# Optimization experiments

Hardware: AMD Instinct MI355X
Metric: run time of the kernel (lower is better)

## Reference

```python
import jax, jax.numpy as jnp
import numpy as np

B, N, H, IN, OUT = 2, 4096, 64, 32, 8


def setup_inputs() -> dict:
    key = jax.random.key(0)
    ks = jax.random.split(key, 18)
    sc = 0.1  # xavier-ish scale for H=64
    mask = lambda k: (jax.random.uniform(k, (1, N, N)) < 0.1).astype(jnp.float32)
    return {
        "x0": jax.random.normal(ks[0], (B, N, IN), jnp.float32),
        "h0": jax.random.normal(ks[1], (B, N, H), jnp.float32),
        "h1": jax.random.normal(ks[2], (B, N, H), jnp.float32),
        "h2": jax.random.normal(ks[3], (B, N, H), jnp.float32),
        "m00": mask(ks[4]), "m20": mask(ks[5]), "m01": mask(ks[6]),
        "m11": mask(ks[7]), "m12": mask(ks[8]), "m22": mask(ks[9]),
        "Wq": jax.random.normal(ks[10], (3, H, H), jnp.float32) * sc,
        "Wk": jax.random.normal(ks[11], (6, H, H), jnp.float32) * sc,
        "Wsu0": jax.random.normal(ks[12], (H, IN + H), jnp.float32) * sc,
        "Wsu12": jax.random.normal(ks[13], (2, H, H), jnp.float32) * sc,
        "Wdt": jax.random.normal(ks[14], (3, H, H), jnp.float32) * sc,
        "bdt": jnp.zeros((3, H), jnp.float32),
        "step_size": jnp.array(1.0, jnp.float32),
        "out_scale": jnp.array(10.0, jnp.float32),
    }


def _cosine_acc(q, keys_and_masks_and_vals):
    # q: [B,N,H]; each entry: (keys [B,Np,H], mask [1,N,Np], vals [B,Np,H])
    qn = q / jnp.linalg.norm(q, axis=2, keepdims=True)
    acc = 0.0
    for k, m, v in keys_and_masks_and_vals:
        kn = k / jnp.linalg.norm(k, axis=2, keepdims=True)
        scale = 1.0 / jnp.sum(m, axis=2, keepdims=True)
        rel = scale * m * jnp.einsum("bnh,bmh->bnm", qn, kn)  # [B,N,Np]
        acc = acc + jnp.einsum("bnm,bmh->bnh", rel, v)
    return acc


def reference(x0, h0, h1, h2, m00, m20, m01, m11, m12, m22,
              Wq, Wk, Wsu0, Wsu12, Wdt, bdt, step_size, out_scale):
    # queries per successor type, keys per edge; edges (pred->succ):
    # 0->0 (k0), 2->0 (k1), 0->1 (k2), 1->1 (k3), 1->2 (k4), 2->2 (k5)
    q0 = h0 @ Wq[0].T
    q1 = h1 @ Wq[1].T
    q2 = h2 @ Wq[2].T
    acc0 = _cosine_acc(q0, [(h0 @ Wk[0].T, m00, h0), (h2 @ Wk[1].T, m20, h2)])
    acc1 = _cosine_acc(q1, [(h0 @ Wk[2].T, m01, h0), (h1 @ Wk[3].T, m11, h1)])
    acc2 = _cosine_acc(q2, [(h1 @ Wk[4].T, m12, h1), (h2 @ Wk[5].T, m22, h2)])

    def step(h, acc_in, Wsu, t):
        dt = 2.0 * jax.nn.sigmoid(h @ Wdt[t].T + bdt[t]) - 1.0
        return h + step_size * dt * (acc_in @ Wsu.T)

    h0n = step(h0, jnp.concatenate([x0, acc0], axis=2), Wsu0, 0)
    h1n = step(h1, acc1, Wsu12[0], 1)
    h2n = step(h2, acc2, Wsu12[1], 2)
    out2 = out_scale * h2n[:, :, :OUT]
    return (out2, h0n, h1n, h2n)
```

## Files before the change

### kernel.cpp

```cpp
#include <hip/hip_runtime.h>

typedef __bf16 bf16;
typedef bf16 bf16x8 __attribute__((ext_vector_type(8)));
typedef float f32x4 __attribute__((ext_vector_type(4)));
typedef unsigned int uint;
typedef uint u32x2 __attribute__((ext_vector_type(2)));
typedef uint u32x4 __attribute__((ext_vector_type(4)));
typedef unsigned short u16x8 __attribute__((ext_vector_type(8)));

constexpr int NT = 4096;

__device__ __forceinline__ bf16x8 ld8f(const float* p) {
    f32x4 a = *(const f32x4*)p;
    f32x4 b = *(const f32x4*)(p + 4);
    bf16x8 v;
    v[0] = (bf16)a[0]; v[1] = (bf16)a[1]; v[2] = (bf16)a[2]; v[3] = (bf16)a[3];
    v[4] = (bf16)b[0]; v[5] = (bf16)b[1]; v[6] = (bf16)b[2]; v[7] = (bf16)b[3];
    return v;
}

__device__ __forceinline__ uint pack2(float a, float b) {
    unsigned short ua = __builtin_bit_cast(unsigned short, (bf16)a);
    unsigned short ub = __builtin_bit_cast(unsigned short, (bf16)b);
    return (uint)ua | ((uint)ub << 16);
}

__global__ __launch_bounds__(256) void prep_kernel(
    const float* __restrict__ h0, const float* __restrict__ h1, const float* __restrict__ h2,
    const float* __restrict__ Wq, const float* __restrict__ Wk,
    const float* __restrict__ m00, const float* __restrict__ m20, const float* __restrict__ m01,
    const float* __restrict__ m11, const float* __restrict__ m12, const float* __restrict__ m22,
    bf16* __restrict__ qn, bf16* __restrict__ kn, bf16* __restrict__ vT,
    uint* __restrict__ mb, float* __restrict__ rs2)
{
    __shared__ __align__(16) unsigned short tlds[4][16][72];
    const int tid = threadIdx.x, wid = tid >> 6, lane = tid & 63;
    const int l15 = lane & 15, quad = lane >> 4;
    const int bx = blockIdx.x;

    if (bx >= 1536) {
        const int mi = bx - 1536;
        const int e = mi >> 10, rb = mi & 1023;
        const int row = rb * 4 + wid;
        const float* masks[6] = {m00, m20, m01, m11, m12, m22};
        const float* mrow = masks[e] + (size_t)row * NT;
        uint lo = 0, hi = 0;
        int cnt = 0;
#pragma unroll 8
        for (int k = 0; k < 64; k++) {
            float m = mrow[64 * k + lane];
            unsigned long long bal = __ballot(m > 0.5f);
            cnt += __popcll(bal);
            if (lane == k) { lo = (uint)bal; hi = (uint)(bal >> 32); }
        }
        if (lane == 0) rs2[e * NT + row] = (float)cnt;
        u32x2 w = {lo, hi};
        ((u32x2*)(mb + (size_t)(e * NT + row) * 128))[lane] = w;
        return;
    }

    const int rt = bx & 127, sl = bx >> 7;
    const int g0 = rt * 64;
    const int grow = g0 + wid * 16 + l15;
    const float* hs[3] = {h0, h1, h2};
    const int predmap[6] = {0, 2, 0, 1, 1, 2};

    if (sl >= 9) {
        const int p = sl - 9;
        bf16x8 af[2];
#pragma unroll
        for (int hc = 0; hc < 2; hc++)
            af[hc] = ld8f(hs[p] + (size_t)grow * 64 + hc * 32 + quad * 8);
#pragma unroll
        for (int hc = 0; hc < 2; hc++)
            *(u16x8*)(&tlds[wid][l15][hc * 32 + quad * 8]) = __builtin_bit_cast(u16x8, af[hc]);
        unsigned short vals[16];
#pragma unroll
        for (int r = 0; r < 16; r++) vals[r] = tlds[wid][r][lane];
        uint us[8];
#pragma unroll
        for (int k = 0; k < 8; k++) us[k] = (uint)vals[2 * k] | ((uint)vals[2 * k + 1] << 16);
        const int gr0 = g0 + wid * 16;
        const int bb = gr0 >> 12, n0 = gr0 & 4095;
        uint* dst = (uint*)(vT + ((size_t)(p * 2 + bb) * 64 + lane) * NT + n0);
        u32x4 w0 = {us[0], us[1], us[2], us[3]};
        u32x4 w1 = {us[4], us[5], us[6], us[7]};
        *(u32x4*)dst = w0;
        *(u32x4*)(dst + 4) = w1;
        return;
    }

    const int pj = sl;
    const float* W = (pj < 3) ? (Wq + pj * 4096) : (Wk + (pj - 3) * 4096);
    const int src = (pj < 3) ? pj : predmap[pj - 3];
    bf16* outp = (pj < 3) ? (qn + (size_t)pj * 2 * NT * 64)
                          : (kn + (size_t)(pj - 3) * 2 * NT * 64);
    bf16x8 af[2];
#pragma unroll
    for (int hc = 0; hc < 2; hc++)
        af[hc] = ld8f(hs[src] + (size_t)grow * 64 + hc * 32 + quad * 8);

    f32x4 s[4];
#pragma unroll
    for (int it = 0; it < 4; it++) {
        f32x4 acc = {0.f, 0.f, 0.f, 0.f};
#pragma unroll
        for (int hc = 0; hc < 2; hc++) {
            bf16x8 wb = ld8f(W + (size_t)(it * 16 + l15) * 64 + hc * 32 + quad * 8);
            acc = __builtin_amdgcn_mfma_f32_16x16x32_bf16(af[hc], wb, acc, 0, 0, 0);
        }
        s[it] = acc;
    }
#pragma unroll
    for (int r = 0; r < 4; r++) {
        float ss = s[0][r] * s[0][r] + s[1][r] * s[1][r] + s[2][r] * s[2][r] + s[3][r] * s[3][r];
        ss += __shfl_xor(ss, 1); ss += __shfl_xor(ss, 2);
        ss += __shfl_xor(ss, 4); ss += __shfl_xor(ss, 8);
        float rn = rsqrtf(ss);
        s[0][r] *= rn; s[1][r] *= rn; s[2][r] *= rn; s[3][r] *= rn;
    }
    const int rowbase = g0 + wid * 16 + quad * 4;
#pragma unroll
    for (int it = 0; it < 4; it++)
#pragma unroll
        for (int r = 0; r < 4; r++)
            outp[(size_t)(rowbase + r) * 64 + it * 16 + l15] = (bf16)s[it][r];
}

template<int JC>
__global__ __launch_bounds__(256, 4) void attn_kernel(
    const bf16* __restrict__ qn, const bf16* __restrict__ kn, const bf16* __restrict__ vT,
    const uint* __restrict__ mb, float* __restrict__ Pacc)
{
    __shared__ __align__(16) bf16 Klds[64][72];
    __shared__ __align__(16) bf16 Vlds[64][72];
    const int tid = threadIdx.x, wid = tid >> 6, lane = tid & 63;
    const int l15 = lane & 15, quad = lane >> 4;
    constexpr int G = 6 * 32 * 2 * JC;
    const int bxr = blockIdx.x;
    const int wg = (bxr & 7) * (G >> 3) + (bxr >> 3);
    const int jcv = wg % JC;
    int r = wg / JC;
    const int b = r & 1; r >>= 1;
    const int qt = r & 31; const int e = r >> 5;
    const int qtypemap[6] = {0, 0, 1, 1, 2, 2};
    const int predmap[6]  = {0, 2, 0, 1, 1, 2};
    const int qtv = qtypemap[e], pv = predmap[e];
    const int qrow0 = qt * 128, wstrip = wid * 32;
    constexpr int JSPAN = NT / JC;
    constexpr int NI = JSPAN / 64;
    const int jbeg = jcv * JSPAN;

    int srow[2], sch[2];
#pragma unroll
    for (int s = 0; s < 2; s++) {
        int u = tid + 256 * s;
        srow[s] = u >> 3; sch[s] = u & 7;
    }
    const bf16* Ksrc = kn + ((size_t)(e * 2 + b) * NT + jbeg) * 64;
    const bf16* Vsrc = vT + (size_t)(pv * 2 + b) * 64 * NT + jbeg;

    bf16x8 Qf[2][2];
#pragma unroll
    for (int mt = 0; mt < 2; mt++)
#pragma unroll
        for (int hc = 0; hc < 2; hc++)
            Qf[mt][hc] = *(const bf16x8*)(qn +
                ((size_t)(qtv * 2 + b) * NT + qrow0 + wstrip + mt * 16 + l15) * 64 +
                hc * 32 + quad * 8);

    f32x4 acc2[4][2];
#pragma unroll
    for (int ht = 0; ht < 4; ht++)
#pragma unroll
        for (int mt = 0; mt < 2; mt++) {
            f32x4 z = {0.f, 0.f, 0.f, 0.f};
            acc2[ht][mt] = z;
        }

    const uint* mbase[2];
#pragma unroll
    for (int mt = 0; mt < 2; mt++)
        mbase[mt] = mb + (size_t)(e * NT + qrow0 + wstrip + mt * 16 + l15) * 128 + (jbeg >> 5);

    u32x4 kreg[2], vreg[2];
#pragma unroll
    for (int s = 0; s < 2; s++) {
        kreg[s] = *(const u32x4*)(Ksrc + (size_t)srow[s] * 64 + sch[s] * 8);
        vreg[s] = *(const u32x4*)(Vsrc + (size_t)srow[s] * NT + sch[s] * 8);
    }
    u32x2 mcur[2], mnxt[2];
#pragma unroll
    for (int mt = 0; mt < 2; mt++) {
        mcur[mt] = *(const u32x2*)(mbase[mt]);
        mnxt[mt] = *(const u32x2*)(mbase[mt] + ((NI > 1) ? 2 : 0));
    }

#pragma unroll 1
    for (int ji = 0; ji < NI; ji++) {
        const int jn = (ji + 1 < NI) ? (ji + 1) * 64 : 0;

        __syncthreads();
#pragma unroll
        for (int s = 0; s < 2; s++) {
            *(u32x4*)(&Klds[srow[s]][sch[s] * 8]) = kreg[s];
            *(u32x4*)(&Vlds[srow[s]][sch[s] * 8]) = vreg[s];
        }
        __syncthreads();

#pragma unroll
        for (int s = 0; s < 2; s++) {
            kreg[s] = *(const u32x4*)(Ksrc + (size_t)(jn + srow[s]) * 64 + sch[s] * 8);
            vreg[s] = *(const u32x4*)(Vsrc + (size_t)srow[s] * NT + jn + sch[s] * 8);
        }
        const int woff2 = (ji + 2 < NI) ? 2 * (ji + 2) : 0;
        u32x2 mtmp[2];
#pragma unroll
        for (int mt = 0; mt < 2; mt++)
            mtmp[mt] = *(const u32x2*)(mbase[mt] + woff2);

        uint Pd[4][2][2];
#pragma unroll
        for (int jt = 0; jt < 4; jt++) {
            bf16x8 aK0 = *(const bf16x8*)(&Klds[jt * 16 + l15][quad * 8]);
            bf16x8 aK1 = *(const bf16x8*)(&Klds[jt * 16 + l15][32 + quad * 8]);
#pragma unroll
            for (int mt = 0; mt < 2; mt++) {
                f32x4 sc = {0.f, 0.f, 0.f, 0.f};
                sc = __builtin_amdgcn_mfma_f32_16x16x32_bf16(aK0, Qf[mt][0], sc, 0, 0, 0);
                sc = __builtin_amdgcn_mfma_f32_16x16x32_bf16(aK1, Qf[mt][1], sc, 0, 0, 0);
                const uint w = (jt < 2) ? mcur[mt].x : mcur[mt].y;
                const int sh = (jt & 1) * 16 + quad * 4;
#pragma unroll
                for (int k = 0; k < 4; k++)
                    sc[k] = ((w >> (sh + k)) & 1u) ? sc[k] : 0.0f;
                Pd[jt][mt][0] = pack2(sc[0], sc[1]);
                Pd[jt][mt][1] = pack2(sc[2], sc[3]);
            }
        }
#pragma unroll
        for (int mt = 0; mt < 2; mt++) { mcur[mt] = mnxt[mt]; mnxt[mt] = mtmp[mt]; }

        uint Bf[2][2][4];
#pragma unroll
        for (int mt = 0; mt < 2; mt++)
#pragma unroll
            for (int c = 0; c < 2; c++)
#pragma unroll
                for (int d = 0; d < 2; d++) {
                    uint x = Pd[2 * c][mt][d];
                    uint y = Pd[2 * c + 1][mt][d];
                    asm("v_permlane32_swap_b32 %0, %1\n\t"
                        "v_permlane16_swap_b32 %0, %1"
                        : "+v"(x), "+v"(y));
                    Bf[mt][c][d]     = x;
                    Bf[mt][c][d + 2] = y;
                }

#pragma unroll
        for (int ht = 0; ht < 4; ht++)
#pragma unroll
            for (int c = 0; c < 2; c++) {
                bf16x8 a = *(const bf16x8*)(&Vlds[ht * 16 + l15][c * 32 + quad * 8]);
#pragma unroll
                for (int mt = 0; mt < 2; mt++) {
                    u32x4 t = {Bf[mt][c][0], Bf[mt][c][1], Bf[mt][c][2], Bf[mt][c][3]};
                    bf16x8 bbv = __builtin_bit_cast(bf16x8, t);
                    acc2[ht][mt] =
                        __builtin_amdgcn_mfma_f32_16x16x32_bf16(a, bbv, acc2[ht][mt], 0, 0, 0);
                }
            }
    }

#pragma unroll
    for (int ht = 0; ht < 4; ht++)
#pragma unroll
        for (int mt = 0; mt < 2; mt++) {
            const int n = qrow0 + wstrip + mt * 16 + l15;
            *(f32x4*)(Pacc + ((((size_t)(jcv * 6 + e) * 2 + b) * NT + n) << 6) +
                      ht * 16 + quad * 4) = acc2[ht][mt];
        }
}

template<int JC>
__global__ __launch_bounds__(256) void update_kernel(
    const float* __restrict__ x0, const float* __restrict__ h0,
    const float* __restrict__ h1, const float* __restrict__ h2,
    const float* __restrict__ Wsu0, const float* __restrict__ Wsu12,
    const float* __restrict__ Wdt, const float* __restrict__ bdt,
    const float* __restrict__ stepp, const float* __restrict__ oscp,
    const float* __restrict__ Pacc, const float* __restrict__ rs2,
    float* __restrict__ dout)
{
    const int tid = threadIdx.x, wid = tid >> 6, lane = tid & 63;
    const int l15 = lane & 15, quad = lane >> 4;
    const int bx = blockIdx.x;
    const int ih = (bx >= 384) ? 1 : 0;
    const int base = bx - ih * 384;
    const int rt = base & 127, t = base >> 7;
    const int g0 = rt * 64;
    const int grow = g0 + wid * 16 + l15;
    const int n = grow & 4095, bb = grow >> 12;
    const float step = *stepp, osc = *oscp;
    const float* hs[3] = {h0, h1, h2};
    const float* __restrict__ ht_base = hs[t];

    bf16x8 afh[2], afacc[2], afx;
#pragma unroll
    for (int hc = 0; hc < 2; hc++)
        afh[hc] = ld8f(ht_base + (size_t)grow * 64 + hc * 32 + quad * 8);
    if (t == 0) afx = ld8f(x0 + (size_t)grow * 32 + quad * 8);

    const float i0 = 1.f / rs2[(size_t)(2 * t) * NT + n];
    const float i1 = 1.f / rs2[(size_t)(2 * t + 1) * NT + n];
#pragma unroll
    for (int hc = 0; hc < 2; hc++) {
        f32x4 S0a = {0.f,0.f,0.f,0.f}, S0b = {0.f,0.f,0.f,0.f};
        f32x4 S1a = {0.f,0.f,0.f,0.f}, S1b = {0.f,0.f,0.f,0.f};
#pragma unroll
        for (int jc = 0; jc < JC; jc++) {
            const float* p0 = Pacc + ((((size_t)(jc * 6 + 2 * t) * 2 + bb) * NT + n) << 6) +
                              hc * 32 + quad * 8;
            const float* p1 = Pacc + ((((size_t)(jc * 6 + 2 * t + 1) * 2 + bb) * NT + n) << 6) +
                              hc * 32 + quad * 8;
            S0a += *(const f32x4*)p0;  S0b += *(const f32x4*)(p0 + 4);
            S1a += *(const f32x4*)p1;  S1b += *(const f32x4*)(p1 + 4);
        }
        bf16x8 v;
#pragma unroll
        for (int j = 0; j < 4; j++) v[j]     = (bf16)(S0a[j] * i0 + S1a[j] * i1);
#pragma unroll
        for (int j = 0; j < 4; j++) v[4 + j] = (bf16)(S0b[j] * i0 + S1b[j] * i1);
        afacc[hc] = v;
    }

#pragma unroll
    for (int ii = 0; ii < 2; ii++) {
        const int it = ih * 2 + ii;
        const float bdtv = bdt[t * 64 + it * 16 + l15];
        f32x4 z = {0.f, 0.f, 0.f, 0.f};
        f32x4 u = {0.f, 0.f, 0.f, 0.f};
#pragma unroll
        for (int hc = 0; hc < 2; hc++) {
            bf16x8 wb = ld8f(Wdt + (size_t)t * 4096 + (size_t)(it * 16 + l15) * 64 + hc * 32 + quad * 8);
            z = __builtin_amdgcn_mfma_f32_16x16x32_bf16(afh[hc], wb, z, 0, 0, 0);
        }
        if (t == 0) {
            bf16x8 w0 = ld8f(Wsu0 + (size_t)(it * 16 + l15) * 96 + quad * 8);
            u = __builtin_amdgcn_mfma_f32_16x16x32_bf16(afx, w0, u, 0, 0, 0);
#pragma unroll
            for (int kc = 0; kc < 2; kc++) {
                bf16x8 wk = ld8f(Wsu0 + (size_t)(it * 16 + l15) * 96 + 32 + kc * 32 + quad * 8);
                u = __builtin_amdgcn_mfma_f32_16x16x32_bf16(afacc[kc], wk, u, 0, 0, 0);
            }
        } else {
#pragma unroll
            for (int kc = 0; kc < 2; kc++) {
                bf16x8 wk = ld8f(Wsu12 + (size_t)(t - 1) * 4096 + (size_t)(it * 16 + l15) * 64 + kc * 32 + quad * 8);
                u = __builtin_amdgcn_mfma_f32_16x16x32_bf16(afacc[kc], wk, u, 0, 0, 0);
            }
        }
        const int colg = it * 16 + l15;
#pragma unroll
        for (int r = 0; r < 4; r++) {
            int row = g0 + wid * 16 + quad * 4 + r;
            float zz = z[r] + bdtv;
            float dtv = 2.f / (1.f + __expf(-zz)) - 1.f;
            float hval = ht_base[(size_t)row * 64 + colg];
            float hn = hval + step * dtv * u[r];
            dout[65536 + (size_t)t * 524288 + (size_t)row * 64 + colg] = hn;
            if (t == 2 && colg < 8)
                dout[(size_t)row * 8 + colg] = osc * hn;
        }
    }
}

extern "C" void kernel_launch(void* const* d_in, const int* in_sizes, int n_in,
                              void* d_out, int out_size, void* d_ws, size_t ws_size,
                              hipStream_t stream) {
    const float* x0   = (const float*)d_in[0];
    const float* h0   = (const float*)d_in[1];
    const float* h1   = (const float*)d_in[2];
    const float* h2   = (const float*)d_in[3];
    const float* m00  = (const float*)d_in[4];
    const float* m20  = (const float*)d_in[5];
    const float* m01  = (const float*)d_in[6];
    const float* m11  = (const float*)d_in[7];
    const float* m12  = (const float*)d_in[8];
    const float* m22  = (const float*)d_in[9];
    const float* Wq   = (const float*)d_in[10];
    const float* Wk   = (const float*)d_in[11];
    const float* Wsu0 = (const float*)d_in[12];
    const float* Wsu12= (const float*)d_in[13];
    const float* Wdt  = (const float*)d_in[14];
    const float* bdt  = (const float*)d_in[15];
    const float* step = (const float*)d_in[16];
    const float* oscl = (const float*)d_in[17];

    bf16* qn  = (bf16*)d_ws;
    bf16* kn  = qn + 1572864;
    bf16* vT  = kn + 3145728;
    uint* mb  = (uint*)(vT + 1572864);
    float* rs2 = (float*)(mb + 3145728);
    float* Pacc = rs2 + 24576;

    auto need = [](size_t jc) { return 25264128 + jc * 12582912; };
    const int JC = (ws_size >= need(4)) ? 4 : ((ws_size >= need(2)) ? 2 : 1);

    prep_kernel<<<7680, 256, 0, stream>>>(h0, h1, h2, Wq, Wk,
                                          m00, m20, m01, m11, m12, m22,
                                          qn, kn, vT, mb, rs2);

    if (JC == 4) {
        attn_kernel<4><<<6 * 32 * 2 * 4, 256, 0, stream>>>(qn, kn, vT, mb, Pacc);
        update_kernel<4><<<768, 256, 0, stream>>>(x0, h0, h1, h2, Wsu0, Wsu12, Wdt, bdt,
                                                  step, oscl, Pacc, rs2, (float*)d_out);
    } else if (JC == 2) {
        attn_kernel<2><<<6 * 32 * 2 * 2, 256, 0, stream>>>(qn, kn, vT, mb, Pacc);
        update_kernel<2><<<768, 256, 0, stream>>>(x0, h0, h1, h2, Wsu0, Wsu12, Wdt, bdt,
                                                  step, oscl, Pacc, rs2, (float*)d_out);
    } else {
        attn_kernel<1><<<6 * 32 * 2 * 1, 256, 0, stream>>>(qn, kn, vT, mb, Pacc);
        update_kernel<1><<<768, 256, 0, stream>>>(x0, h0, h1, h2, Wsu0, Wsu12, Wdt, bdt,
                                                  step, oscl, Pacc, rs2, (float*)d_out);
    }
}
```

Before: 481.5 us.

## Widen attention warp tile to 64 query rows and vectorize mask packing

The attention kernel now runs 128-thread blocks with two waves, each covering 64 query rows instead of 32. Each K/V LDS fragment is therefore reused across four MFMA row tiles, halving LDS reads per MFMA but raising register pressure and lowering waves per block. The mask bit layout is changed to match a new per-lane bit ordering. The prep kernel now reads masks as float4 and issues four ballots per iteration, cutting the load count per row, with bit extraction remapped to that layout.

```diff
diff --git a/kernel.cpp b/kernel.cpp
--- a/kernel.cpp
+++ b/kernel.cpp
@@ -44,14 +44,20 @@
         const int row = rb * 4 + wid;
         const float* masks[6] = {m00, m20, m01, m11, m12, m22};
         const float* mrow = masks[e] + (size_t)row * NT;
-        uint lo = 0, hi = 0;
-        int cnt = 0;
+        uint lo = 0, hi = 0, cnt = 0;
+        const int own_it = lane >> 2;
+        const uint s = (uint)(lane & 3) * 16;
 #pragma unroll 8
-        for (int k = 0; k < 64; k++) {
-            float m = mrow[64 * k + lane];
-            unsigned long long bal = __ballot(m > 0.5f);
-            cnt += __popcll(bal);
-            if (lane == k) { lo = (uint)bal; hi = (uint)(bal >> 32); }
+        for (int it = 0; it < 16; it++) {
+            f32x4 v = *(const f32x4*)(mrow + 256 * it + 4 * lane);
+            unsigned long long b0 = __ballot(v[0] > 0.5f);
+            unsigned long long b1 = __ballot(v[1] > 0.5f);
+            unsigned long long b2 = __ballot(v[2] > 0.5f);
+            unsigned long long b3 = __ballot(v[3] > 0.5f);
+            cnt += __popcll(b0) + __popcll(b1) + __popcll(b2) + __popcll(b3);
+            uint locand = ((uint)(b0 >> s) & 0xFFFFu) | (((uint)(b1 >> s) & 0xFFFFu) << 16);
+            uint hicand = ((uint)(b2 >> s) & 0xFFFFu) | (((uint)(b3 >> s) & 0xFFFFu) << 16);
+            if (own_it == it) { lo = locand; hi = hicand; }
         }
         if (lane == 0) rs2[e * NT + row] = (float)cnt;
         u32x2 w = {lo, hi};
@@ -128,7 +134,7 @@
 }
 
 template<int JC>
-__global__ __launch_bounds__(256, 4) void attn_kernel(
+__global__ __launch_bounds__(128, 2) void attn_kernel(
     const bf16* __restrict__ qn, const bf16* __restrict__ kn, const bf16* __restrict__ vT,
     const uint* __restrict__ mb, float* __restrict__ Pacc)
 {
@@ -146,52 +152,52 @@
     const int qtypemap[6] = {0, 0, 1, 1, 2, 2};
     const int predmap[6]  = {0, 2, 0, 1, 1, 2};
     const int qtv = qtypemap[e], pv = predmap[e];
-    const int qrow0 = qt * 128, wstrip = wid * 32;
+    const int qrow0 = qt * 128, wstrip = wid * 64;
     constexpr int JSPAN = NT / JC;
     constexpr int NI = JSPAN / 64;
     const int jbeg = jcv * JSPAN;
 
-    int srow[2], sch[2];
-#pragma unroll
-    for (int s = 0; s < 2; s++) {
-        int u = tid + 256 * s;
+    int srow[4], sch[4];
+#pragma unroll
+    for (int s = 0; s < 4; s++) {
+        int u = tid + 128 * s;
         srow[s] = u >> 3; sch[s] = u & 7;
     }
     const bf16* Ksrc = kn + ((size_t)(e * 2 + b) * NT + jbeg) * 64;
     const bf16* Vsrc = vT + (size_t)(pv * 2 + b) * 64 * NT + jbeg;
 
-    bf16x8 Qf[2][2];
-#pragma unroll
-    for (int mt = 0; mt < 2; mt++)
+    bf16x8 Qf[4][2];
+#pragma unroll
+    for (int mt = 0; mt < 4; mt++)
 #pragma unroll
         for (int hc = 0; hc < 2; hc++)
             Qf[mt][hc] = *(const bf16x8*)(qn +
                 ((size_t)(qtv * 2 + b) * NT + qrow0 + wstrip + mt * 16 + l15) * 64 +
                 hc * 32 + quad * 8);
 
-    f32x4 acc2[4][2];
+    f32x4 acc2[4][4];
 #pragma unroll
     for (int ht = 0; ht < 4; ht++)
 #pragma unroll
-        for (int mt = 0; mt < 2; mt++) {
+        for (int mt = 0; mt < 4; mt++) {
             f32x4 z = {0.f, 0.f, 0.f, 0.f};
             acc2[ht][mt] = z;
         }
 
-    const uint* mbase[2];
-#pragma unroll
-    for (int mt = 0; mt < 2; mt++)
+    const uint* mbase[4];
+#pragma unroll
+    for (int mt = 0; mt < 4; mt++)
         mbase[mt] = mb + (size_t)(e * NT + qrow0 + wstrip + mt * 16 + l15) * 128 + (jbeg >> 5);
 
-    u32x4 kreg[2], vreg[2];
-#pragma unroll
-    for (int s = 0; s < 2; s++) {
+    u32x4 kreg[4], vreg[4];
+#pragma unroll
+    for (int s = 0; s < 4; s++) {
         kreg[s] = *(const u32x4*)(Ksrc + (size_t)srow[s] * 64 + sch[s] * 8);
         vreg[s] = *(const u32x4*)(Vsrc + (size_t)srow[s] * NT + sch[s] * 8);
     }
-    u32x2 mcur[2], mnxt[2];
-#pragma unroll
-    for (int mt = 0; mt < 2; mt++) {
+    u32x2 mcur[4], mnxt[4];
+#pragma unroll
+    for (int mt = 0; mt < 4; mt++) {
         mcur[mt] = *(const u32x2*)(mbase[mt]);
         mnxt[mt] = *(const u32x2*)(mbase[mt] + ((NI > 1) ? 2 : 0));
     }
@@ -202,60 +208,61 @@
 
         __syncthreads();
 #pragma unroll
-        for (int s = 0; s < 2; s++) {
+        for (int s = 0; s < 4; s++) {
             *(u32x4*)(&Klds[srow[s]][sch[s] * 8]) = kreg[s];
             *(u32x4*)(&Vlds[srow[s]][sch[s] * 8]) = vreg[s];
         }
         __syncthreads();
 
 #pragma unroll
-        for (int s = 0; s < 2; s++) {
+        for (int s = 0; s < 4; s++) {
             kreg[s] = *(const u32x4*)(Ksrc + (size_t)(jn + srow[s]) * 64 + sch[s] * 8);
             vreg[s] = *(const u32x4*)(Vsrc + (size_t)srow[s] * NT + jn + sch[s] * 8);
         }
         const int woff2 = (ji + 2 < NI) ? 2 * (ji + 2) : 0;
-        u32x2 mtmp[2];
-#pragma unroll
-        for (int mt = 0; mt < 2; mt++)
+        u32x2 mtmp[4];
+#pragma unroll
+        for (int mt = 0; mt < 4; mt++)
             mtmp[mt] = *(const u32x2*)(mbase[mt] + woff2);
 
-        uint Pd[4][2][2];
+        bf16x8 aK[4][2];
 #pragma unroll
         for (int jt = 0; jt < 4; jt++) {
-            bf16x8 aK0 = *(const bf16x8*)(&Klds[jt * 16 + l15][quad * 8]);
-            bf16x8 aK1 = *(const bf16x8*)(&Klds[jt * 16 + l15][32 + quad * 8]);
-#pragma unroll
-            for (int mt = 0; mt < 2; mt++) {
+            aK[jt][0] = *(const bf16x8*)(&Klds[jt * 16 + l15][quad * 8]);
+            aK[jt][1] = *(const bf16x8*)(&Klds[jt * 16 + l15][32 + quad * 8]);
+        }
+        uint Bf[4][2][4];
+#pragma unroll
+        for (int mt = 0; mt < 4; mt++) {
+            uint Pd[4][2];
+#pragma unroll
+            for (int jt = 0; jt < 4; jt++) {
                 f32x4 sc = {0.f, 0.f, 0.f, 0.f};
-                sc = __builtin_amdgcn_mfma_f32_16x16x32_bf16(aK0, Qf[mt][0], sc, 0, 0, 0);
-                sc = __builtin_amdgcn_mfma_f32_16x16x32_bf16(aK1, Qf[mt][1], sc, 0, 0, 0);
-                const uint w = (jt < 2) ? mcur[mt].x : mcur[mt].y;
-                const int sh = (jt & 1) * 16 + quad * 4;
-#pragma unroll
-                for (int k = 0; k < 4; k++)
-                    sc[k] = ((w >> (sh + k)) & 1u) ? sc[k] : 0.0f;
-                Pd[jt][mt][0] = pack2(sc[0], sc[1]);
-                Pd[jt][mt][1] = pack2(sc[2], sc[3]);
+                sc = __builtin_amdgcn_mfma_f32_16x16x32_bf16(aK[jt][0], Qf[mt][0], sc, 0, 0, 0);
+                sc = __builtin_amdgcn_mfma_f32_16x16x32_bf16(aK[jt][1], Qf[mt][1], sc, 0, 0, 0);
+#pragma unroll
+                for (int k = 0; k < 4; k++) {
+                    const uint w = (k < 2) ? mcur[mt].x : mcur[mt].y;
+                    sc[k] = ((w >> ((k & 1) * 16 + jt * 4 + quad)) & 1u) ? sc[k] : 0.0f;
+                }
+                Pd[jt][0] = pack2(sc[0], sc[1]);
+                Pd[jt][1] = pack2(sc[2], sc[3]);
             }
-        }
-#pragma unroll
-        for (int mt = 0; mt < 2; mt++) { mcur[mt] = mnxt[mt]; mnxt[mt] = mtmp[mt]; }
-
-        uint Bf[2][2][4];
-#pragma unroll
-        for (int mt = 0; mt < 2; mt++)
 #pragma unroll
             for (int c = 0; c < 2; c++)
 #pragma unroll
                 for (int d = 0; d < 2; d++) {
-                    uint x = Pd[2 * c][mt][d];
-                    uint y = Pd[2 * c + 1][mt][d];
+                    uint x = Pd[2 * c][d];
+                    uint y = Pd[2 * c + 1][d];
                     asm("v_permlane32_swap_b32 %0, %1\n\t"
                         "v_permlane16_swap_b32 %0, %1"
                         : "+v"(x), "+v"(y));
                     Bf[mt][c][d]     = x;
                     Bf[mt][c][d + 2] = y;
                 }
+        }
+#pragma unroll
+        for (int mt = 0; mt < 4; mt++) { mcur[mt] = mnxt[mt]; mnxt[mt] = mtmp[mt]; }
 
 #pragma unroll
         for (int ht = 0; ht < 4; ht++)
@@ -263,7 +270,7 @@
             for (int c = 0; c < 2; c++) {
                 bf16x8 a = *(const bf16x8*)(&Vlds[ht * 16 + l15][c * 32 + quad * 8]);
 #pragma unroll
-                for (int mt = 0; mt < 2; mt++) {
+                for (int mt = 0; mt < 4; mt++) {
                     u32x4 t = {Bf[mt][c][0], Bf[mt][c][1], Bf[mt][c][2], Bf[mt][c][3]};
                     bf16x8 bbv = __builtin_bit_cast(bf16x8, t);
                     acc2[ht][mt] =
@@ -275,7 +282,7 @@
 #pragma unroll
     for (int ht = 0; ht < 4; ht++)
 #pragma unroll
-        for (int mt = 0; mt < 2; mt++) {
+        for (int mt = 0; mt < 4; mt++) {
             const int n = qrow0 + wstrip + mt * 16 + l15;
             *(f32x4*)(Pacc + ((((size_t)(jcv * 6 + e) * 2 + b) * NT + n) << 6) +
                       ht * 16 + quad * 4) = acc2[ht][mt];
@@ -412,15 +419,15 @@
                                           qn, kn, vT, mb, rs2);
 
     if (JC == 4) {
-        attn_kernel<4><<<6 * 32 * 2 * 4, 256, 0, stream>>>(qn, kn, vT, mb, Pacc);
+        attn_kernel<4><<<6 * 32 * 2 * 4, 128, 0, stream>>>(qn, kn, vT, mb, Pacc);
         update_kernel<4><<<768, 256, 0, stream>>>(x0, h0, h1, h2, Wsu0, Wsu12, Wdt, bdt,
                                                   step, oscl, Pacc, rs2, (float*)d_out);
     } else if (JC == 2) {
-        attn_kernel<2><<<6 * 32 * 2 * 2, 256, 0, stream>>>(qn, kn, vT, mb, Pacc);
+        attn_kernel<2><<<6 * 32 * 2 * 2, 128, 0, stream>>>(qn, kn, vT, mb, Pacc);
         update_kernel<2><<<768, 256, 0, stream>>>(x0, h0, h1, h2, Wsu0, Wsu12, Wdt, bdt,
                                                   step, oscl, Pacc, rs2, (float*)d_out);
     } else {
-        attn_kernel<1><<<6 * 32 * 2 * 1, 256, 0, stream>>>(qn, kn, vT, mb, Pacc);
+        attn_kernel<1><<<6 * 32 * 2 * 1, 128, 0, stream>>>(qn, kn, vT, mb, Pacc);
         update_kernel<1><<<768, 256, 0, stream>>>(x0, h0, h1, h2, Wsu0, Wsu12, Wdt, bdt,
                                                   step, oscl, Pacc, rs2, (float*)d_out);
     }
```

Result: slower. 508.9 us (+5.7%).

## Split mask packing into vectorized kernel and double-buffer K/V LDS in attention

Applied to the files above, without the earlier changes.

Mask bit-packing moves out of prep_kernel into a separate mask_kernel. That kernel loads float4 per lane with a 4-deep register prefetch and builds a new interleaved bit layout from four ballots per step. The attention kernel now double-buffers its K/V LDS tiles, cutting from two barriers per iteration to one, and its mask-bit indexing is changed to match the new packing. The intent is to raise memory throughput on the 400MB mask read and to reduce barrier stalls in attention. The cost is one extra kernel launch and twice the LDS use in attention, which may lower occupancy.

```diff
diff --git a/kernel.cpp b/kernel.cpp
--- a/kernel.cpp
+++ b/kernel.cpp
@@ -25,40 +25,54 @@
     return (uint)ua | ((uint)ub << 16);
 }
 
+__global__ __launch_bounds__(256) void mask_kernel(
+    const float* __restrict__ m00, const float* __restrict__ m20, const float* __restrict__ m01,
+    const float* __restrict__ m11, const float* __restrict__ m12, const float* __restrict__ m22,
+    uint* __restrict__ mb, float* __restrict__ rs2)
+{
+    const int tid = threadIdx.x, wid = tid >> 6, lane = tid & 63;
+    const int mi = blockIdx.x;
+    const int e = mi >> 10, rb = mi & 1023;
+    const int row = rb * 4 + wid;
+    const float* masks[6] = {m00, m20, m01, m11, m12, m22};
+    const float* mrow = masks[e] + (size_t)row * NT;
+    const int own_it = lane >> 2;
+    const uint s = (uint)(lane & 3) * 16;
+
+    f32x4 buf[4];
+#pragma unroll
+    for (int p = 0; p < 4; p++)
+        buf[p] = *(const f32x4*)(mrow + 256 * p + 4 * lane);
+
+    uint lo = 0, hi = 0, cnt = 0;
+#pragma unroll
+    for (int it = 0; it < 16; it++) {
+        f32x4 v = buf[it & 3];
+        if (it + 4 < 16)
+            buf[it & 3] = *(const f32x4*)(mrow + 256 * (it + 4) + 4 * lane);
+        unsigned long long b0 = __ballot(v[0] > 0.5f);
+        unsigned long long b1 = __ballot(v[1] > 0.5f);
+        unsigned long long b2 = __ballot(v[2] > 0.5f);
+        unsigned long long b3 = __ballot(v[3] > 0.5f);
+        cnt += __popcll(b0) + __popcll(b1) + __popcll(b2) + __popcll(b3);
+        uint locand = ((uint)(b0 >> s) & 0xFFFFu) | (((uint)(b1 >> s) & 0xFFFFu) << 16);
+        uint hicand = ((uint)(b2 >> s) & 0xFFFFu) | (((uint)(b3 >> s) & 0xFFFFu) << 16);
+        if (own_it == it) { lo = locand; hi = hicand; }
+    }
+    if (lane == 0) rs2[e * NT + row] = (float)cnt;
+    u32x2 w = {lo, hi};
+    ((u32x2*)(mb + (size_t)(e * NT + row) * 128))[lane] = w;
+}
+
 __global__ __launch_bounds__(256) void prep_kernel(
     const float* __restrict__ h0, const float* __restrict__ h1, const float* __restrict__ h2,
     const float* __restrict__ Wq, const float* __restrict__ Wk,
-    const float* __restrict__ m00, const float* __restrict__ m20, const float* __restrict__ m01,
-    const float* __restrict__ m11, const float* __restrict__ m12, const float* __restrict__ m22,
-    bf16* __restrict__ qn, bf16* __restrict__ kn, bf16* __restrict__ vT,
-    uint* __restrict__ mb, float* __restrict__ rs2)
+    bf16* __restrict__ qn, bf16* __restrict__ kn, bf16* __restrict__ vT)
 {
     __shared__ __align__(16) unsigned short tlds[4][16][72];
     const int tid = threadIdx.x, wid = tid >> 6, lane = tid & 63;
     const int l15 = lane & 15, quad = lane >> 4;
     const int bx = blockIdx.x;
-
-    if (bx >= 1536) {
-        const int mi = bx - 1536;
-        const int e = mi >> 10, rb = mi & 1023;
-        const int row = rb * 4 + wid;
-        const float* masks[6] = {m00, m20, m01, m11, m12, m22};
-        const float* mrow = masks[e] + (size_t)row * NT;
-        uint lo = 0, hi = 0;
-        int cnt = 0;
-#pragma unroll 8
-        for (int k = 0; k < 64; k++) {
-            float m = mrow[64 * k + lane];
-            unsigned long long bal = __ballot(m > 0.5f);
-            cnt += __popcll(bal);
-            if (lane == k) { lo = (uint)bal; hi = (uint)(bal >> 32); }
-        }
-        if (lane == 0) rs2[e * NT + row] = (float)cnt;
-        u32x2 w = {lo, hi};
-        ((u32x2*)(mb + (size_t)(e * NT + row) * 128))[lane] = w;
-        return;
-    }
-
     const int rt = bx & 127, sl = bx >> 7;
     const int g0 = rt * 64;
     const int grow = g0 + wid * 16 + l15;
@@ -132,8 +146,8 @@
     const bf16* __restrict__ qn, const bf16* __restrict__ kn, const bf16* __restrict__ vT,
     const uint* __restrict__ mb, float* __restrict__ Pacc)
 {
-    __shared__ __align__(16) bf16 Klds[64][72];
-    __shared__ __align__(16) bf16 Vlds[64][72];
+    __shared__ __align__(16) bf16 Klds[2][64][72];
+    __shared__ __align__(16) bf16 Vlds[2][64][72];
     const int tid = threadIdx.x, wid = tid >> 6, lane = tid & 63;
     const int l15 = lane & 15, quad = lane >> 4;
     constexpr int G = 6 * 32 * 2 * JC;
@@ -195,24 +209,24 @@
         mcur[mt] = *(const u32x2*)(mbase[mt]);
         mnxt[mt] = *(const u32x2*)(mbase[mt] + ((NI > 1) ? 2 : 0));
     }
+#pragma unroll
+    for (int s = 0; s < 2; s++) {
+        *(u32x4*)(&Klds[0][srow[s]][sch[s] * 8]) = kreg[s];
+        *(u32x4*)(&Vlds[0][srow[s]][sch[s] * 8]) = vreg[s];
+    }
+    {
+        const int j1 = (NI > 1) ? 64 : 0;
+#pragma unroll
+        for (int s = 0; s < 2; s++) {
+            kreg[s] = *(const u32x4*)(Ksrc + (size_t)(j1 + srow[s]) * 64 + sch[s] * 8);
+            vreg[s] = *(const u32x4*)(Vsrc + (size_t)srow[s] * NT + j1 + sch[s] * 8);
+        }
+    }
+    __syncthreads();
 
 #pragma unroll 1
     for (int ji = 0; ji < NI; ji++) {
-        const int jn = (ji + 1 < NI) ? (ji + 1) * 64 : 0;
-
-        __syncthreads();
-#pragma unroll
-        for (int s = 0; s < 2; s++) {
-            *(u32x4*)(&Klds[srow[s]][sch[s] * 8]) = kreg[s];
-            *(u32x4*)(&Vlds[srow[s]][sch[s] * 8]) = vreg[s];
-        }
-        __syncthreads();
-
-#pragma unroll
-        for (int s = 0; s < 2; s++) {
-            kreg[s] = *(const u32x4*)(Ksrc + (size_t)(jn + srow[s]) * 64 + sch[s] * 8);
-            vreg[s] = *(const u32x4*)(Vsrc + (size_t)srow[s] * NT + jn + sch[s] * 8);
-        }
+        const int cur = ji & 1;
         const int woff2 = (ji + 2 < NI) ? 2 * (ji + 2) : 0;
         u32x2 mtmp[2];
 #pragma unroll
@@ -222,18 +236,18 @@
         uint Pd[4][2][2];
 #pragma unroll
         for (int jt = 0; jt < 4; jt++) {
-            bf16x8 aK0 = *(const bf16x8*)(&Klds[jt * 16 + l15][quad * 8]);
-            bf16x8 aK1 = *(const bf16x8*)(&Klds[jt * 16 + l15][32 + quad * 8]);
+            bf16x8 aK0 = *(const bf16x8*)(&Klds[cur][jt * 16 + l15][quad * 8]);
+            bf16x8 aK1 = *(const bf16x8*)(&Klds[cur][jt * 16 + l15][32 + quad * 8]);
 #pragma unroll
             for (int mt = 0; mt < 2; mt++) {
                 f32x4 sc = {0.f, 0.f, 0.f, 0.f};
                 sc = __builtin_amdgcn_mfma_f32_16x16x32_bf16(aK0, Qf[mt][0], sc, 0, 0, 0);
                 sc = __builtin_amdgcn_mfma_f32_16x16x32_bf16(aK1, Qf[mt][1], sc, 0, 0, 0);
-                const uint w = (jt < 2) ? mcur[mt].x : mcur[mt].y;
-                const int sh = (jt & 1) * 16 + quad * 4;
-#pragma unroll
-                for (int k = 0; k < 4; k++)
-                    sc[k] = ((w >> (sh + k)) & 1u) ? sc[k] : 0.0f;
+#pragma unroll
+                for (int k = 0; k < 4; k++) {
+                    const uint w = (k < 2) ? mcur[mt].x : mcur[mt].y;
+                    sc[k] = ((w >> ((k & 1) * 16 + jt * 4 + quad)) & 1u) ? sc[k] : 0.0f;
+                }
                 Pd[jt][mt][0] = pack2(sc[0], sc[1]);
                 Pd[jt][mt][1] = pack2(sc[2], sc[3]);
             }
@@ -261,7 +275,7 @@
         for (int ht = 0; ht < 4; ht++)
 #pragma unroll
             for (int c = 0; c < 2; c++) {
-                bf16x8 a = *(const bf16x8*)(&Vlds[ht * 16 + l15][c * 32 + quad * 8]);
+                bf16x8 a = *(const bf16x8*)(&Vlds[cur][ht * 16 + l15][c * 32 + quad * 8]);
 #pragma unroll
                 for (int mt = 0; mt < 2; mt++) {
                     u32x4 t = {Bf[mt][c][0], Bf[mt][c][1], Bf[mt][c][2], Bf[mt][c][3]};
@@ -270,6 +284,22 @@
                         __builtin_amdgcn_mfma_f32_16x16x32_bf16(a, bbv, acc2[ht][mt], 0, 0, 0);
                 }
             }
+
+        if (ji + 1 < NI) {
+            const int nxt = cur ^ 1;
+#pragma unroll
+            for (int s = 0; s < 2; s++) {
+                *(u32x4*)(&Klds[nxt][srow[s]][sch[s] * 8]) = kreg[s];
+                *(u32x4*)(&Vlds[nxt][srow[s]][sch[s] * 8]) = vreg[s];
+            }
+            const int j2 = (ji + 2 < NI) ? (ji + 2) * 64 : 0;
+#pragma unroll
+            for (int s = 0; s < 2; s++) {
+                kreg[s] = *(const u32x4*)(Ksrc + (size_t)(j2 + srow[s]) * 64 + sch[s] * 8);
+                vreg[s] = *(const u32x4*)(Vsrc + (size_t)srow[s] * NT + j2 + sch[s] * 8);
+            }
+            __syncthreads();
+        }
     }
 
 #pragma unroll
@@ -407,9 +437,8 @@
     auto need = [](size_t jc) { return 25264128 + jc * 12582912; };
     const int JC = (ws_size >= need(4)) ? 4 : ((ws_size >= need(2)) ? 2 : 1);
 
-    prep_kernel<<<7680, 256, 0, stream>>>(h0, h1, h2, Wq, Wk,
-                                          m00, m20, m01, m11, m12, m22,
-                                          qn, kn, vT, mb, rs2);
+    mask_kernel<<<6144, 256, 0, stream>>>(m00, m20, m01, m11, m12, m22, mb, rs2);
+    prep_kernel<<<1536, 256, 0, stream>>>(h0, h1, h2, Wq, Wk, qn, kn, vT);
 
     if (JC == 4) {
         attn_kernel<4><<<6 * 32 * 2 * 4, 256, 0, stream>>>(qn, kn, vT, mb, Pacc);
```

Measured after the change: 482.1 us. Within noise of the previous version (+0.1%).
